# Kernel tuning notes

Hardware: AMD Instinct MI355X
Metric: run time of the kernel (lower is better)

## Reference

```python
import jax, jax.numpy as jnp
import numpy as np

B, T, F, H = 256, 512, 64, 128


def _uniform(key, shape, stdv):
    return jax.random.uniform(key, shape, jnp.float32, -stdv, stdv)


def setup_inputs() -> dict:
    key = jax.random.key(0)
    ks = jax.random.split(key, 24)
    values = jax.random.normal(ks[0], (B, T, F), jnp.float32)
    masks = (jax.random.uniform(ks[1], (B, T, F)) < 0.8).astype(jnp.float32)
    deltas = jax.random.uniform(ks[2], (B, T, F), jnp.float32)
    labels = (jax.random.uniform(ks[3], (B, 1)) < 0.5).astype(jnp.float32)
    is_train = (jax.random.uniform(ks[4], (B, 1)) < 0.8).astype(jnp.float32)
    sH = 1.0 / np.sqrt(H)
    sF = 1.0 / np.sqrt(F)
    # temp_decay_h: Linear F -> H (stdv = 1/sqrt(out) per reset_parameters)
    W_dh = _uniform(ks[5], (H, F), sH); b_dh = _uniform(ks[6], (H,), sH)
    # temp_decay_x: diag F -> F
    W_dx = _uniform(ks[7], (F, F), sF); b_dx = _uniform(ks[8], (F,), sF)
    # hist_reg: Linear H -> F (torch Linear stdv = 1/sqrt(in))
    W_hr = _uniform(ks[9], (F, H), sH); b_hr = _uniform(ks[10], (F,), sH)
    # feat_reg: F -> F with zeroed diagonal mask
    W_fr = _uniform(ks[11], (F, F), sF); b_fr = _uniform(ks[12], (F,), sF)
    # weight_combine: Linear 2F -> F
    s2F = 1.0 / np.sqrt(2 * F)
    W_wc = _uniform(ks[13], (F, 2 * F), s2F); b_wc = _uniform(ks[14], (F,), s2F)
    # LSTMCell(2F, H): torch init uniform(-1/sqrt(H), 1/sqrt(H)), gate order i,f,g,o
    W_ih = _uniform(ks[15], (4 * H, 2 * F), sH); b_ih = _uniform(ks[16], (4 * H,), sH)
    W_hh = _uniform(ks[17], (4 * H, H), sH); b_hh = _uniform(ks[18], (4 * H,), sH)
    # out: Linear H -> 1
    W_out = _uniform(ks[19], (1, H), sH); b_out = _uniform(ks[20], (1,), sH)
    return dict(values=values, masks=masks, deltas=deltas, labels=labels, is_train=is_train,
                W_dh=W_dh, b_dh=b_dh, W_dx=W_dx, b_dx=b_dx, W_hr=W_hr, b_hr=b_hr,
                W_fr=W_fr, b_fr=b_fr, W_wc=W_wc, b_wc=b_wc,
                W_ih=W_ih, b_ih=b_ih, W_hh=W_hh, b_hh=b_hh, W_out=W_out, b_out=b_out)


def _forward(values, masks, deltas, labels, is_train,
             W_dh, b_dh, W_dx, b_dx, W_hr, b_hr, W_fr, b_fr, W_wc, b_wc,
             W_ih, b_ih, W_hh, b_hh, W_out, b_out):
    eps = 1e-5
    w_dx_diag = jnp.diagonal(W_dx)            # diag mask: W * I
    W_fr_m = W_fr * (1.0 - jnp.eye(F, dtype=W_fr.dtype))  # zero diagonal

    def step(carry, xs):
        h, c, x_loss = carry
        x, m, d = xs                           # each [B, F]
        gamma_h = jnp.exp(-jax.nn.relu(d @ W_dh.T + b_dh))   # [B, H]
        gamma_x = jnp.exp(-jax.nn.relu(d * w_dx_diag + b_dx))  # [B, F]
        h = h * gamma_h
        x_h = h @ W_hr.T + b_hr                # [B, F]
        msum = jnp.sum(m) + eps
        x_loss = x_loss + jnp.sum(jnp.abs(x - x_h) * m) / msum
        x_c = m * x + (1.0 - m) * x_h
        z_h = x_c @ W_fr_m.T + b_fr
        x_loss = x_loss + jnp.sum(jnp.abs(x - z_h) * m) / msum
        alpha = jnp.concatenate([gamma_x, m], axis=1) @ W_wc.T + b_wc
        c_h = alpha * z_h + (1.0 - alpha) * x_h
        x_loss = x_loss + jnp.sum(jnp.abs(x - c_h) * m) / msum
        c_c = m * x + (1.0 - m) * c_h
        inp = jnp.concatenate([c_c, m], axis=1)   # [B, 2F]
        gates = inp @ W_ih.T + b_ih + h @ W_hh.T + b_hh  # [B, 4H]
        i, f, g, o = jnp.split(gates, 4, axis=1)
        c = jax.nn.sigmoid(f) * c + jax.nn.sigmoid(i) * jnp.tanh(g)
        h = jax.nn.sigmoid(o) * jnp.tanh(c)
        return (h, c, x_loss), c_c

    h0 = jnp.zeros((values.shape[0], H), values.dtype)
    c0 = jnp.zeros((values.shape[0], H), values.dtype)
    xs = (jnp.swapaxes(values, 0, 1), jnp.swapaxes(masks, 0, 1), jnp.swapaxes(deltas, 0, 1))
    (h, c, x_loss), imps = jax.lax.scan(step, (h0, c0, jnp.float32(0.0)), xs)
    imputations = jnp.swapaxes(imps, 0, 1)     # [B, T, F]
    y_h = h @ W_out.T + b_out                  # [B, 1] logits
    # stable BCE with logits (matches torch reference formula)
    max_val = jnp.maximum(-y_h, 0.0)
    y_l = y_h - y_h * labels + max_val + jnp.log(jnp.exp(-max_val) + jnp.exp(-y_h - max_val))
    y_loss = jnp.sum(y_l * is_train) / (jnp.sum(is_train) + eps)
    loss = x_loss / T + y_loss * 0.3
    predictions = jax.nn.sigmoid(y_h)
    return loss, predictions, imputations


def reference(values, masks, deltas, labels, is_train,
              W_dh, b_dh, W_dx, b_dx, W_hr, b_hr, W_fr, b_fr, W_wc, b_wc,
              W_ih, b_ih, W_hh, b_hh, W_out, b_out):
    return _forward(values, masks, deltas, labels, is_train,
                    W_dh, b_dh, W_dx, b_dx, W_hr, b_hr, W_fr, b_fr, W_wc, b_wc,
                    W_ih, b_ih, W_hh, b_hh, W_out, b_out)
```

## Files before the change

### kernel.cpp

```cpp
#include <hip/hip_runtime.h>
#include <hip/hip_fp16.h>


#define NBATCH 256
#define NT 512
#define NF 64
#define NH 128

#define WHH_OFF   0u
#define WIH_OFF   131072u
#define WHR_OFF   262144u
#define WFR_OFF   278528u
#define INVMS_OFF 286720u
#define ISTR_OFF  288768u
#define GH_OFF    294912u
#define AL_OFF    33849344u

typedef _Float16 half2_t __attribute__((ext_vector_type(2)));

__device__ __forceinline__ unsigned pack2(float a, float b) {
    __half2 h = __floats2half2_rn(a, b);
    return __builtin_bit_cast(unsigned, h);
}

__device__ __forceinline__ float dot2f(unsigned w, unsigned a, float acc) {
#if __has_builtin(__builtin_amdgcn_fdot2)
    return __builtin_amdgcn_fdot2(__builtin_bit_cast(half2_t, w),
                                  __builtin_bit_cast(half2_t, a), acc, false);
#else
    float2 wf = __half22float2(__builtin_bit_cast(__half2, w));
    float2 af = __half22float2(__builtin_bit_cast(__half2, a));
    return acc + wf.x * af.x + wf.y * af.y;
#endif
}

__device__ __forceinline__ float sigm(float x) { return 1.f / (1.f + __expf(-x)); }
__device__ __forceinline__ float tanh_fast(float x) { return 1.f - 2.f / (__expf(2.f * x) + 1.f); }

__global__ __launch_bounds__(256) void prep_w(const float* __restrict__ Whh,
                                              const float* __restrict__ Wih,
                                              const float* __restrict__ Whr,
                                              const float* __restrict__ Wfr,
                                              unsigned* __restrict__ wsu) {
    int o = blockIdx.x * 256 + threadIdx.x;
    float v0, v1;
    if (o < 32768) {
        int c = o & 3, r = (o >> 2) & 511, cb = o >> 11;
        int col = 8 * cb + 2 * c;
        v0 = Whh[r * 128 + col]; v1 = Whh[r * 128 + col + 1];
    } else if (o < 65536) {
        int o2 = o - 32768;
        int c = o2 & 3, r = (o2 >> 2) & 511, cb = o2 >> 11;
        int col = 8 * cb + 2 * c;
        v0 = Wih[r * 128 + col]; v1 = Wih[r * 128 + col + 1];
    } else if (o < 69632) {
        int o3 = o - 65536;
        int c = o3 & 3, f = (o3 >> 2) & 63, cb = o3 >> 8;
        int col = 8 * cb + 2 * c;
        v0 = Whr[f * 128 + col]; v1 = Whr[f * 128 + col + 1];
    } else if (o < 71680) {
        int o4 = o - 69632;
        int c = o4 & 3, f = (o4 >> 2) & 63, cb = o4 >> 8;
        int col = 8 * cb + 2 * c;
        v0 = (col == f) ? 0.f : Wfr[f * 64 + col];
        v1 = (col + 1 == f) ? 0.f : Wfr[f * 64 + col + 1];
    } else {
        return;
    }
    wsu[o] = pack2(v0, v1);
}

__global__ __launch_bounds__(256) void prep_msum(const float* __restrict__ masks,
                                                 const float* __restrict__ is_train,
                                                 float* __restrict__ invms,
                                                 float* __restrict__ inv_istr,
                                                 float* __restrict__ d_out0) {
    __shared__ float red[256];
    int tid = threadIdx.x;
    int t = blockIdx.x;
    if (t < NT) {
        int f = tid & 63, br = tid >> 6;
        float s = 0.f;
        for (int i = 0; i < 64; i++) {
            int b = br + i * 4;
            s += masks[((size_t)b * NT + t) * NF + f];
        }
        red[tid] = s;
        __syncthreads();
        for (int off = 128; off > 0; off >>= 1) {
            if (tid < off) red[tid] += red[tid + off];
            __syncthreads();
        }
        if (tid == 0) invms[t] = 1.f / (red[0] + 1e-5f);
    } else {
        red[tid] = is_train[tid];
        __syncthreads();
        for (int off = 128; off > 0; off >>= 1) {
            if (tid < off) red[tid] += red[tid + off];
            __syncthreads();
        }
        if (tid == 0) {
            *inv_istr = 1.f / (red[0] + 1e-5f);
            *d_out0 = 0.f;
        }
    }
}

__global__ __launch_bounds__(256) void ga_kernel(const float* __restrict__ deltas,
                                                 const float* __restrict__ masks,
                                                 const float* __restrict__ Wdh,
                                                 const float* __restrict__ bdh,
                                                 const float* __restrict__ Wdx,
                                                 const float* __restrict__ bdx,
                                                 const float* __restrict__ Wwc,
                                                 const float* __restrict__ bwc,
                                                 __half* __restrict__ gh_all,
                                                 __half* __restrict__ al_all) {
    __shared__ unsigned wdhpk[32 * 128];
    __shared__ unsigned wwcpk[64 * 64];
    __shared__ float sbdh[128], sbdx[64], swdx[64], sbwc[64];
    __shared__ float dbuf[64];
    __shared__ __align__(16) unsigned dpk[32], gxpk[32], mpk2[32];
    int tid = threadIdx.x;

    for (int o = tid; o < 4096; o += 256) {
        int j = o & 127, k2 = o >> 7;
        wdhpk[o] = pack2(Wdh[j * 64 + 2 * k2], Wdh[j * 64 + 2 * k2 + 1]);
    }
    for (int o = tid; o < 4096; o += 256) {
        int f = o & 63, k2 = o >> 6;
        wwcpk[o] = pack2(Wwc[f * 128 + 2 * k2], Wwc[f * 128 + 2 * k2 + 1]);
    }
    if (tid < 128) sbdh[tid] = bdh[tid];
    if (tid < 64) {
        sbdx[tid] = bdx[tid];
        swdx[tid] = Wdx[tid * 65];
        sbwc[tid] = bwc[tid];
    }
    __syncthreads();

    for (int i = 0; i < 32; i++) {
        int p = blockIdx.x * 32 + i;
        if (tid < 32) {
            float2 dv = ((const float2*)(deltas + (size_t)p * NF))[tid];
            dbuf[2 * tid] = dv.x; dbuf[2 * tid + 1] = dv.y;
            dpk[tid] = pack2(dv.x, dv.y);
        } else if (tid < 64) {
            int q = tid - 32;
            float2 mv = ((const float2*)(masks + (size_t)p * NF))[q];
            mpk2[q] = pack2(mv.x, mv.y);
        }
        __syncthreads();
        if (tid < 64) {
            float gx = __expf(-fmaxf(dbuf[tid] * swdx[tid] + sbdx[tid], 0.f));
            float oth = __shfl_xor(gx, 1);
            if (!(tid & 1)) gxpk[tid >> 1] = pack2(gx, oth);
        }
        __syncthreads();
        if (tid < 128) {
            float a0 = sbdh[tid], a1 = 0.f;
            #pragma unroll
            for (int k8 = 0; k8 < 8; k8++) {
                uint4 dp = *(const uint4*)&dpk[4 * k8];
                a0 = dot2f(wdhpk[(4 * k8 + 0) * 128 + tid], dp.x, a0);
                a1 = dot2f(wdhpk[(4 * k8 + 1) * 128 + tid], dp.y, a1);
                a0 = dot2f(wdhpk[(4 * k8 + 2) * 128 + tid], dp.z, a0);
                a1 = dot2f(wdhpk[(4 * k8 + 3) * 128 + tid], dp.w, a1);
            }
            gh_all[(size_t)p * NH + tid] = __float2half(__expf(-fmaxf(a0 + a1, 0.f)));
        } else if (tid < 192) {
            int f = tid - 128;
            float a0 = sbwc[f], a1 = 0.f;
            #pragma unroll
            for (int k8 = 0; k8 < 8; k8++) {
                uint4 gp = *(const uint4*)&gxpk[4 * k8];
                a0 = dot2f(wwcpk[(4 * k8 + 0) * 64 + f], gp.x, a0);
                a1 = dot2f(wwcpk[(4 * k8 + 1) * 64 + f], gp.y, a1);
                a0 = dot2f(wwcpk[(4 * k8 + 2) * 64 + f], gp.z, a0);
                a1 = dot2f(wwcpk[(4 * k8 + 3) * 64 + f], gp.w, a1);
            }
            #pragma unroll
            for (int k8 = 0; k8 < 8; k8++) {
                uint4 mp = *(const uint4*)&mpk2[4 * k8];
                a0 = dot2f(wwcpk[(32 + 4 * k8 + 0) * 64 + f], mp.x, a0);
                a1 = dot2f(wwcpk[(32 + 4 * k8 + 1) * 64 + f], mp.y, a1);
                a0 = dot2f(wwcpk[(32 + 4 * k8 + 2) * 64 + f], mp.z, a0);
                a1 = dot2f(wwcpk[(32 + 4 * k8 + 3) * 64 + f], mp.w, a1);
            }
            al_all[(size_t)p * NF + f] = __float2half(a0 + a1);
        }
        __syncthreads();
    }
}

__global__ __launch_bounds__(512, 2) void main_kernel(
    const float* __restrict__ values, const float* __restrict__ masks,
    const float* __restrict__ labels, const float* __restrict__ is_train,
    const float* __restrict__ b_hr, const float* __restrict__ b_fr,
    const float* __restrict__ b_ih, const float* __restrict__ b_hh,
    const float* __restrict__ W_out, const float* __restrict__ b_out,
    const uint4* __restrict__ whh_ws, const uint4* __restrict__ wih_ws,
    const uint4* __restrict__ whr_ws, const uint4* __restrict__ wfr_ws,
    const float* __restrict__ invms, const float* __restrict__ inv_istr,
    const __half* __restrict__ gh_all, const __half* __restrict__ al_all,
    float* __restrict__ d_out) {
    __shared__ uint4 whr4[16 * 64];
    __shared__ uint4 wfr4[8 * 64];
    __shared__ float bgate[512];
    __shared__ float sbhr[64], sbfr[64];
    __shared__ float hbuf[128], cbuf[128];
    __shared__ float mbuf[64];
    __shared__ __align__(16) unsigned hpk[64];
    __shared__ __align__(16) unsigned mpk[32], xcpk[32], ccpk[32];
    __shared__ float gates[512];

    const int tid = threadIdx.x;
    const int b = blockIdx.x;

    uint4 whh_r[16], wih_r[16];
    #pragma unroll
    for (int cb = 0; cb < 16; cb++) {
        whh_r[cb] = whh_ws[cb * 512 + tid];
        wih_r[cb] = wih_ws[cb * 512 + tid];
    }
    for (int o = tid; o < 1024; o += 512) whr4[o] = whr_ws[o];
    if (tid < 512) wfr4[tid] = wfr_ws[tid];
    bgate[tid] = b_ih[tid] + b_hh[tid];
    if (tid < 64) { sbhr[tid] = b_hr[tid]; sbfr[tid] = b_fr[tid]; }
    if (tid < 128) { hbuf[tid] = 0.f; cbuf[tid] = 0.f; }
    if (tid < 64) hpk[tid] = 0u;

    const float* vp = values + (size_t)b * NT * NF;
    const float* mp = masks + (size_t)b * NT * NF;
    const __half* alp = al_all + (size_t)b * NT * NF;
    const unsigned* ghu = (const unsigned*)(gh_all + (size_t)b * NT * NH);
    float* imp = d_out + 257 + (size_t)b * NT * NF;

    float lloss = 0.f;
    float xreg = 0.f, mreg = 0.f, xh_reg = 0.f;

    float xn = 0.f, aln = 0.f, invtn = 0.f;
    float2 mn = make_float2(0.f, 0.f);
    unsigned ghn = 0u;
    float alc = 0.f, invtc = 0.f;

    if (tid < 64) {
        xn = vp[tid];
        aln = __half2float(alp[tid]);
        invtn = invms[0];
    } else if (tid < 96) {
        mn = ((const float2*)mp)[tid - 64];
    } else if (tid < 160) {
        ghn = ghu[tid - 96];
    }
    __syncthreads();

    for (int t = 0; t < NT; t++) {
        if (tid < 64) {
            xreg = xn; alc = aln; invtc = invtn;
        } else if (tid < 96) {
            int q = tid - 64;
            mbuf[2 * q] = mn.x; mbuf[2 * q + 1] = mn.y;
            mpk[q] = pack2(mn.x, mn.y);
        } else if (tid < 160) {
            int q = tid - 96;
            float2 g = __half22float2(__builtin_bit_cast(__half2, ghn));
            float h0 = hbuf[2 * q] * g.x;
            float h1 = hbuf[2 * q + 1] * g.y;
            hbuf[2 * q] = h0; hbuf[2 * q + 1] = h1;
            hpk[q] = pack2(h0, h1);
        }
        __syncthreads();

        if (tid < 64) {
            int f = tid;
            mreg = mbuf[f];
            float a0 = sbhr[f], a1 = 0.f;
            #pragma unroll
            for (int k4 = 0; k4 < 16; k4 += 2) {
                uint4 w = whr4[k4 * 64 + f];
                uint4 hp = *(const uint4*)&hpk[4 * k4];
                a0 = dot2f(w.x, hp.x, a0); a0 = dot2f(w.y, hp.y, a0);
                a0 = dot2f(w.z, hp.z, a0); a0 = dot2f(w.w, hp.w, a0);
                uint4 w2 = whr4[(k4 + 1) * 64 + f];
                uint4 hp2 = *(const uint4*)&hpk[4 * k4 + 4];
                a1 = dot2f(w2.x, hp2.x, a1); a1 = dot2f(w2.y, hp2.y, a1);
                a1 = dot2f(w2.z, hp2.z, a1); a1 = dot2f(w2.w, hp2.w, a1);
            }
            xh_reg = a0 + a1;
            float xc = mreg * xreg + (1.f - mreg) * xh_reg;
            float oth = __shfl_xor(xc, 1);
            if (!(f & 1)) xcpk[f >> 1] = pack2(xc, oth);
        }
        __syncthreads();

        if (tid < 64) {
            int f = tid;
            float a0 = sbfr[f], a1 = 0.f;
            #pragma unroll
            for (int k4 = 0; k4 < 8; k4++) {
                uint4 w = wfr4[k4 * 64 + f];
                uint4 xp = *(const uint4*)&xcpk[4 * k4];
                a0 = dot2f(w.x, xp.x, a0); a1 = dot2f(w.y, xp.y, a1);
                a0 = dot2f(w.z, xp.z, a0); a1 = dot2f(w.w, xp.w, a1);
            }
            float zh = a0 + a1;
            float ch = alc * zh + (1.f - alc) * xh_reg;
            float cc = mreg * xreg + (1.f - mreg) * ch;
            imp[t * NF + f] = cc;
            lloss += (fabsf(xreg - xh_reg) + fabsf(xreg - zh) + fabsf(xreg - ch)) * mreg * invtc;
            float oth = __shfl_xor(cc, 1);
            if (!(f & 1)) ccpk[f >> 1] = pack2(cc, oth);
        }
        __syncthreads();

        {
            int tn = (t + 1 < NT) ? (t + 1) : (NT - 1);
            if (tid < 64) {
                xn = vp[tn * NF + tid];
                aln = __half2float(alp[tn * NF + tid]);
                invtn = invms[tn];
            } else if (tid < 96) {
                mn = ((const float2*)(mp + tn * NF))[tid - 64];
            } else if (tid < 160) {
                ghn = ghu[(size_t)tn * 64 + (tid - 96)];
            }

            float a0 = bgate[tid], a1 = 0.f, a2 = 0.f, a3 = 0.f;
            #pragma unroll
            for (int cb = 0; cb < 8; cb++) {
                uint4 ap = *(const uint4*)&ccpk[4 * cb];
                uint4 w = wih_r[cb];
                a0 = dot2f(w.x, ap.x, a0); a1 = dot2f(w.y, ap.y, a1);
                a2 = dot2f(w.z, ap.z, a2); a3 = dot2f(w.w, ap.w, a3);
            }
            #pragma unroll
            for (int cb = 0; cb < 8; cb++) {
                uint4 ap = *(const uint4*)&mpk[4 * cb];
                uint4 w = wih_r[8 + cb];
                a0 = dot2f(w.x, ap.x, a0); a1 = dot2f(w.y, ap.y, a1);
                a2 = dot2f(w.z, ap.z, a2); a3 = dot2f(w.w, ap.w, a3);
            }
            #pragma unroll
            for (int k4 = 0; k4 < 16; k4++) {
                uint4 hp = *(const uint4*)&hpk[4 * k4];
                uint4 w = whh_r[k4];
                a0 = dot2f(w.x, hp.x, a0); a1 = dot2f(w.y, hp.y, a1);
                a2 = dot2f(w.z, hp.z, a2); a3 = dot2f(w.w, hp.w, a3);
            }
            gates[tid] = (a0 + a1) + (a2 + a3);
        }
        __syncthreads();

        if (tid < 128) {
            float gi = gates[tid], gf = gates[128 + tid];
            float gg = gates[256 + tid], go = gates[384 + tid];
            float cn = sigm(gf) * cbuf[tid] + sigm(gi) * tanh_fast(gg);
            cbuf[tid] = cn;
            hbuf[tid] = sigm(go) * tanh_fast(cn);
        }
        __syncthreads();
    }

    if (tid < 64) {
        float ll = lloss;
        float yp = hbuf[tid] * W_out[tid] + hbuf[64 + tid] * W_out[64 + tid];
        #pragma unroll
        for (int off = 32; off > 0; off >>= 1) {
            ll += __shfl_down(ll, off);
            yp += __shfl_down(yp, off);
        }
        if (tid == 0) {
            float yh = yp + b_out[0];
            d_out[1 + b] = 1.f / (1.f + expf(-yh));
            float lab = labels[b], istr = is_train[b];
            float maxv = fmaxf(-yh, 0.f);
            float yl = yh - yh * lab + maxv + logf(expf(-maxv) + expf(-yh - maxv));
            atomicAdd(d_out, ll * (1.f / (float)NT) + 0.3f * yl * istr * (*inv_istr));
        }
    }
}

extern "C" void kernel_launch(void* const* d_in, const int* in_sizes, int n_in,
                              void* d_out, int out_size, void* d_ws, size_t ws_size,
                              hipStream_t stream) {
    const float* values = (const float*)d_in[0];
    const float* masks = (const float*)d_in[1];
    const float* deltas = (const float*)d_in[2];
    const float* labels = (const float*)d_in[3];
    const float* is_train = (const float*)d_in[4];
    const float* W_dh = (const float*)d_in[5];
    const float* b_dh = (const float*)d_in[6];
    const float* W_dx = (const float*)d_in[7];
    const float* b_dx = (const float*)d_in[8];
    const float* W_hr = (const float*)d_in[9];
    const float* b_hr = (const float*)d_in[10];
    const float* W_fr = (const float*)d_in[11];
    const float* b_fr = (const float*)d_in[12];
    const float* W_wc = (const float*)d_in[13];
    const float* b_wc = (const float*)d_in[14];
    const float* W_ih = (const float*)d_in[15];
    const float* b_ih = (const float*)d_in[16];
    const float* W_hh = (const float*)d_in[17];
    const float* b_hh = (const float*)d_in[18];
    const float* W_out = (const float*)d_in[19];
    const float* b_out = (const float*)d_in[20];

    char* ws = (char*)d_ws;
    unsigned* wsu = (unsigned*)d_ws;
    const uint4* whh_ws = (const uint4*)(ws + WHH_OFF);
    const uint4* wih_ws = (const uint4*)(ws + WIH_OFF);
    const uint4* whr_ws = (const uint4*)(ws + WHR_OFF);
    const uint4* wfr_ws = (const uint4*)(ws + WFR_OFF);
    float* invms = (float*)(ws + INVMS_OFF);
    float* inv_istr = (float*)(ws + ISTR_OFF);
    __half* gh_all = (__half*)(ws + GH_OFF);
    __half* al_all = (__half*)(ws + AL_OFF);
    float* out_f = (float*)d_out;

    prep_w<<<280, 256, 0, stream>>>(W_hh, W_ih, W_hr, W_fr, wsu);
    prep_msum<<<513, 256, 0, stream>>>(masks, is_train, invms, inv_istr, out_f);
    ga_kernel<<<4096, 256, 0, stream>>>(deltas, masks, W_dh, b_dh, W_dx, b_dx,
                                        W_wc, b_wc, gh_all, al_all);
    main_kernel<<<NBATCH, 512, 0, stream>>>(values, masks, labels, is_train,
                                            b_hr, b_fr, b_ih, b_hh, W_out, b_out,
                                            whh_ws, wih_ws, whr_ws, wfr_ws,
                                            invms, inv_istr, gh_all, al_all, out_f);
}
```

Baseline: 1.376 ms.

## Compute LSTM gates with MFMA and split regression dot products across all threads

The LSTM gate matrix-vector product, previously done with per-thread fdot2 over register-resident weights, now uses 16x16x32 f16 MFMA instructions. The combined W_ih|W_hh weights are pre-swizzled into A-fragment layout so they can stay in registers. The hidden-state part of the gates is issued early to overlap with the regression stages. The hist_reg and feat_reg dot products are split across all 8 waves, with partial sums reduced in shared memory at the cost of an extra barrier. Cell state moves into registers, the decayed h is packed directly, next-step loads are prefetched at loop top, and ga_kernel gets more blocks with fewer positions each.

```diff
diff --git a/kernel.cpp b/kernel.cpp
--- a/kernel.cpp
+++ b/kernel.cpp
@@ -7,8 +7,7 @@
 #define NF 64
 #define NH 128
 
-#define WHH_OFF   0u
-#define WIH_OFF   131072u
+#define AFRAG_OFF 0u
 #define WHR_OFF   262144u
 #define WFR_OFF   278528u
 #define INVMS_OFF 286720u
@@ -17,6 +16,8 @@
 #define AL_OFF    33849344u
 
 typedef _Float16 half2_t __attribute__((ext_vector_type(2)));
+typedef _Float16 half8_t __attribute__((ext_vector_type(8)));
+typedef float float4_t __attribute__((ext_vector_type(4)));
 
 __device__ __forceinline__ unsigned pack2(float a, float b) {
     __half2 h = __floats2half2_rn(a, b);
@@ -34,25 +35,31 @@
 #endif
 }
 
+__device__ __forceinline__ float4_t mfma16(half8_t a, half8_t b, float4_t c) {
+    return __builtin_amdgcn_mfma_f32_16x16x32_f16(a, b, c, 0, 0, 0);
+}
+
 __device__ __forceinline__ float sigm(float x) { return 1.f / (1.f + __expf(-x)); }
 __device__ __forceinline__ float tanh_fast(float x) { return 1.f - 2.f / (__expf(2.f * x) + 1.f); }
 
-__global__ __launch_bounds__(256) void prep_w(const float* __restrict__ Whh,
-                                              const float* __restrict__ Wih,
+__global__ __launch_bounds__(256) void prep_w(const float* __restrict__ Wih,
+                                              const float* __restrict__ Whh,
                                               const float* __restrict__ Whr,
                                               const float* __restrict__ Wfr,
                                               unsigned* __restrict__ wsu) {
     int o = blockIdx.x * 256 + threadIdx.x;
     float v0, v1;
-    if (o < 32768) {
-        int c = o & 3, r = (o >> 2) & 511, cb = o >> 11;
-        int col = 8 * cb + 2 * c;
-        v0 = Whh[r * 128 + col]; v1 = Whh[r * 128 + col + 1];
-    } else if (o < 65536) {
-        int o2 = o - 32768;
-        int c = o2 & 3, r = (o2 >> 2) & 511, cb = o2 >> 11;
-        int col = 8 * cb + 2 * c;
-        v0 = Wih[r * 128 + col]; v1 = Wih[r * 128 + col + 1];
+    if (o < 65536) {
+        int comp = o & 3;
+        int u4 = o >> 2;
+        int lane = u4 & 63;
+        int tile = u4 >> 6;
+        int kt = tile & 7, rt = (tile >> 3) & 3, w = tile >> 5;
+        int row = 64 * w + 16 * rt + (lane & 15);
+        int kp = 16 * kt + ((lane >> 4) << 2) + comp;
+        int k0 = 2 * kp;
+        if (k0 < 128) { v0 = Wih[row * 128 + k0]; v1 = Wih[row * 128 + k0 + 1]; }
+        else          { v0 = Whh[row * 128 + k0 - 128]; v1 = Whh[row * 128 + k0 - 127]; }
     } else if (o < 69632) {
         int o3 = o - 65536;
         int c = o3 & 3, f = (o3 >> 2) & 63, cb = o3 >> 8;
@@ -139,8 +146,8 @@
     }
     __syncthreads();
 
-    for (int i = 0; i < 32; i++) {
-        int p = blockIdx.x * 32 + i;
+    for (int i = 0; i < 8; i++) {
+        int p = blockIdx.x * 8 + i;
         if (tid < 32) {
             float2 dv = ((const float2*)(deltas + (size_t)p * NF))[tid];
             dbuf[2 * tid] = dv.x; dbuf[2 * tid + 1] = dv.y;
@@ -199,172 +206,196 @@
     const float* __restrict__ b_hr, const float* __restrict__ b_fr,
     const float* __restrict__ b_ih, const float* __restrict__ b_hh,
     const float* __restrict__ W_out, const float* __restrict__ b_out,
-    const uint4* __restrict__ whh_ws, const uint4* __restrict__ wih_ws,
-    const uint4* __restrict__ whr_ws, const uint4* __restrict__ wfr_ws,
+    const uint4* __restrict__ afrag_ws, const uint4* __restrict__ whr_ws,
+    const uint4* __restrict__ wfr_ws,
     const float* __restrict__ invms, const float* __restrict__ inv_istr,
     const __half* __restrict__ gh_all, const __half* __restrict__ al_all,
     float* __restrict__ d_out) {
-    __shared__ uint4 whr4[16 * 64];
-    __shared__ uint4 wfr4[8 * 64];
-    __shared__ float bgate[512];
+    __shared__ __align__(16) uint4 whr4u[16 * 64];
+    __shared__ __align__(16) uint4 wfr4u[8 * 64];
+    __shared__ float bpart[512], cpart[512], gates[512];
+    __shared__ float xbuf[64], mbuf[64], albuf[64];
     __shared__ float sbhr[64], sbfr[64];
-    __shared__ float hbuf[128], cbuf[128];
-    __shared__ float mbuf[64];
     __shared__ __align__(16) unsigned hpk[64];
     __shared__ __align__(16) unsigned mpk[32], xcpk[32], ccpk[32];
-    __shared__ float gates[512];
+    __shared__ float sinv[1];
 
     const int tid = threadIdx.x;
     const int b = blockIdx.x;
-
-    uint4 whh_r[16], wih_r[16];
+    const int f = tid & 63;
+    const int s = tid >> 6;
+    const int q4 = (tid >> 4) & 3;
+
+    uint4 afr[4][8];
     #pragma unroll
-    for (int cb = 0; cb < 16; cb++) {
-        whh_r[cb] = whh_ws[cb * 512 + tid];
-        wih_r[cb] = wih_ws[cb * 512 + tid];
-    }
-    for (int o = tid; o < 1024; o += 512) whr4[o] = whr_ws[o];
-    if (tid < 512) wfr4[tid] = wfr_ws[tid];
-    bgate[tid] = b_ih[tid] + b_hh[tid];
+    for (int rt = 0; rt < 4; rt++)
+        #pragma unroll
+        for (int kt = 0; kt < 8; kt++) {
+            afr[rt][kt] = afrag_ws[(((s * 4 + rt) * 8) + kt) * 64 + f];
+            asm volatile("" : "+v"(afr[rt][kt].x), "+v"(afr[rt][kt].y),
+                              "+v"(afr[rt][kt].z), "+v"(afr[rt][kt].w));
+        }
+
+    float4_t bias_r[4];
+    #pragma unroll
+    for (int rt = 0; rt < 4; rt++)
+        #pragma unroll
+        for (int reg = 0; reg < 4; reg++) {
+            int row = 64 * s + 16 * rt + 4 * q4 + reg;
+            bias_r[rt][reg] = b_ih[row] + b_hh[row];
+        }
+
+    for (int o = tid; o < 1024; o += 512) whr4u[o] = whr_ws[o];
+    if (tid < 512) wfr4u[tid] = wfr_ws[tid];
     if (tid < 64) { sbhr[tid] = b_hr[tid]; sbfr[tid] = b_fr[tid]; }
-    if (tid < 128) { hbuf[tid] = 0.f; cbuf[tid] = 0.f; }
-    if (tid < 64) hpk[tid] = 0u;
 
     const float* vp = values + (size_t)b * NT * NF;
     const float* mp = masks + (size_t)b * NT * NF;
     const __half* alp = al_all + (size_t)b * NT * NF;
-    const unsigned* ghu = (const unsigned*)(gh_all + (size_t)b * NT * NH);
+    const __half* ghp = gh_all + (size_t)b * NT * NH;
     float* imp = d_out + 257 + (size_t)b * NT * NF;
 
+    if (tid < 64) {
+        float x0 = vp[tid];
+        float m0 = mp[tid];
+        xbuf[tid] = x0; mbuf[tid] = m0;
+        albuf[tid] = __half2float(alp[tid]);
+        float m1 = __shfl_xor(m0, 1);
+        if (!(tid & 1)) mpk[tid >> 1] = pack2(m0, m1);
+        hpk[tid] = 0u;
+    }
+    if (tid == 64) sinv[0] = invms[0];
+    __syncthreads();
+
+    float creg = 0.f, hn = 0.f;
     float lloss = 0.f;
-    float xreg = 0.f, mreg = 0.f, xh_reg = 0.f;
-
-    float xn = 0.f, aln = 0.f, invtn = 0.f;
-    float2 mn = make_float2(0.f, 0.f);
-    unsigned ghn = 0u;
-    float alc = 0.f, invtc = 0.f;
-
-    if (tid < 64) {
-        xn = vp[tid];
-        aln = __half2float(alp[tid]);
-        invtn = invms[0];
-    } else if (tid < 96) {
-        mn = ((const float2*)mp)[tid - 64];
-    } else if (tid < 160) {
-        ghn = ghu[tid - 96];
-    }
-    __syncthreads();
 
     for (int t = 0; t < NT; t++) {
+        int tn = (t + 1 < NT) ? (t + 1) : (NT - 1);
+        __half ghn = __float2half(0.f);
+        float2 mn2 = make_float2(0.f, 0.f);
+        float xn = 0.f, aln = 0.f, invtn = 0.f;
+        if (tid < 128) ghn = ghp[(size_t)tn * NH + tid];
+        else if (tid < 160) mn2 = ((const float2*)(mp + tn * NF))[tid - 128];
+        else if (tid < 256 && tid >= 192) xn = vp[tn * NF + (tid - 192)];
+        else if (tid >= 256 && tid < 320) aln = __half2float(alp[tn * NF + (tid - 256)]);
+        else if (tid == 320) invtn = invms[tn];
+
+        float4_t acc[4];
+        {
+            half8_t bh[4];
+            #pragma unroll
+            for (int j = 0; j < 4; j++)
+                bh[j] = *((const half8_t*)&hpk[16 * j + 4 * q4]);
+            #pragma unroll
+            for (int rt = 0; rt < 4; rt++) {
+                acc[rt] = bias_r[rt];
+                #pragma unroll
+                for (int j = 0; j < 4; j++)
+                    acc[rt] = mfma16(__builtin_bit_cast(half8_t, afr[rt][4 + j]), bh[j], acc[rt]);
+            }
+        }
+
+        {
+            uint4 w0 = whr4u[(2 * s) * 64 + f];
+            uint4 w1 = whr4u[(2 * s + 1) * 64 + f];
+            uint4 h0 = *(const uint4*)&hpk[8 * s];
+            uint4 h1 = *(const uint4*)&hpk[8 * s + 4];
+            float p0 = 0.f, p1 = 0.f;
+            p0 = dot2f(w0.x, h0.x, p0); p1 = dot2f(w0.y, h0.y, p1);
+            p0 = dot2f(w0.z, h0.z, p0); p1 = dot2f(w0.w, h0.w, p1);
+            p0 = dot2f(w1.x, h1.x, p0); p1 = dot2f(w1.y, h1.y, p1);
+            p0 = dot2f(w1.z, h1.z, p0); p1 = dot2f(w1.w, h1.w, p1);
+            bpart[s * 64 + f] = p0 + p1;
+        }
+        __syncthreads();
+
+        float xreg = 0.f, mreg = 0.f, invt = 0.f, xh_keep = 0.f;
         if (tid < 64) {
-            xreg = xn; alc = aln; invtc = invtn;
-        } else if (tid < 96) {
-            int q = tid - 64;
-            mbuf[2 * q] = mn.x; mbuf[2 * q + 1] = mn.y;
-            mpk[q] = pack2(mn.x, mn.y);
-        } else if (tid < 160) {
-            int q = tid - 96;
-            float2 g = __half22float2(__builtin_bit_cast(__half2, ghn));
-            float h0 = hbuf[2 * q] * g.x;
-            float h1 = hbuf[2 * q + 1] * g.y;
-            hbuf[2 * q] = h0; hbuf[2 * q + 1] = h1;
-            hpk[q] = pack2(h0, h1);
-        }
-        __syncthreads();
-
-        if (tid < 64) {
-            int f = tid;
-            mreg = mbuf[f];
-            float a0 = sbhr[f], a1 = 0.f;
-            #pragma unroll
-            for (int k4 = 0; k4 < 16; k4 += 2) {
-                uint4 w = whr4[k4 * 64 + f];
-                uint4 hp = *(const uint4*)&hpk[4 * k4];
-                a0 = dot2f(w.x, hp.x, a0); a0 = dot2f(w.y, hp.y, a0);
-                a0 = dot2f(w.z, hp.z, a0); a0 = dot2f(w.w, hp.w, a0);
-                uint4 w2 = whr4[(k4 + 1) * 64 + f];
-                uint4 hp2 = *(const uint4*)&hpk[4 * k4 + 4];
-                a1 = dot2f(w2.x, hp2.x, a1); a1 = dot2f(w2.y, hp2.y, a1);
-                a1 = dot2f(w2.z, hp2.z, a1); a1 = dot2f(w2.w, hp2.w, a1);
-            }
-            xh_reg = a0 + a1;
-            float xc = mreg * xreg + (1.f - mreg) * xh_reg;
+            float xh = sbhr[f];
+            #pragma unroll
+            for (int s2 = 0; s2 < 8; s2++) xh += bpart[s2 * 64 + f];
+            xreg = xbuf[f]; mreg = mbuf[f]; invt = sinv[0];
+            xh_keep = xh;
+            float xc = mreg * xreg + (1.f - mreg) * xh;
+            lloss += fabsf(xreg - xh) * mreg * invt;
             float oth = __shfl_xor(xc, 1);
             if (!(f & 1)) xcpk[f >> 1] = pack2(xc, oth);
         }
         __syncthreads();
 
+        {
+            uint4 w = wfr4u[s * 64 + f];
+            uint4 xp = *(const uint4*)&xcpk[4 * s];
+            float p0 = 0.f, p1 = 0.f;
+            p0 = dot2f(w.x, xp.x, p0); p1 = dot2f(w.y, xp.y, p1);
+            p0 = dot2f(w.z, xp.z, p0); p1 = dot2f(w.w, xp.w, p1);
+            cpart[s * 64 + f] = p0 + p1;
+        }
+        __syncthreads();
+
         if (tid < 64) {
-            int f = tid;
-            float a0 = sbfr[f], a1 = 0.f;
-            #pragma unroll
-            for (int k4 = 0; k4 < 8; k4++) {
-                uint4 w = wfr4[k4 * 64 + f];
-                uint4 xp = *(const uint4*)&xcpk[4 * k4];
-                a0 = dot2f(w.x, xp.x, a0); a1 = dot2f(w.y, xp.y, a1);
-                a0 = dot2f(w.z, xp.z, a0); a1 = dot2f(w.w, xp.w, a1);
-            }
-            float zh = a0 + a1;
-            float ch = alc * zh + (1.f - alc) * xh_reg;
+            float zh = sbfr[f];
+            #pragma unroll
+            for (int s2 = 0; s2 < 8; s2++) zh += cpart[s2 * 64 + f];
+            float al = albuf[f];
+            float ch = al * zh + (1.f - al) * xh_keep;
             float cc = mreg * xreg + (1.f - mreg) * ch;
             imp[t * NF + f] = cc;
-            lloss += (fabsf(xreg - xh_reg) + fabsf(xreg - zh) + fabsf(xreg - ch)) * mreg * invtc;
+            lloss += (fabsf(xreg - zh) + fabsf(xreg - ch)) * mreg * invt;
             float oth = __shfl_xor(cc, 1);
             if (!(f & 1)) ccpk[f >> 1] = pack2(cc, oth);
         }
         __syncthreads();
 
         {
-            int tn = (t + 1 < NT) ? (t + 1) : (NT - 1);
-            if (tid < 64) {
-                xn = vp[tn * NF + tid];
-                aln = __half2float(alp[tn * NF + tid]);
-                invtn = invms[tn];
-            } else if (tid < 96) {
-                mn = ((const float2*)(mp + tn * NF))[tid - 64];
-            } else if (tid < 160) {
-                ghn = ghu[(size_t)tn * 64 + (tid - 96)];
-            }
-
-            float a0 = bgate[tid], a1 = 0.f, a2 = 0.f, a3 = 0.f;
-            #pragma unroll
-            for (int cb = 0; cb < 8; cb++) {
-                uint4 ap = *(const uint4*)&ccpk[4 * cb];
-                uint4 w = wih_r[cb];
-                a0 = dot2f(w.x, ap.x, a0); a1 = dot2f(w.y, ap.y, a1);
-                a2 = dot2f(w.z, ap.z, a2); a3 = dot2f(w.w, ap.w, a3);
-            }
-            #pragma unroll
-            for (int cb = 0; cb < 8; cb++) {
-                uint4 ap = *(const uint4*)&mpk[4 * cb];
-                uint4 w = wih_r[8 + cb];
-                a0 = dot2f(w.x, ap.x, a0); a1 = dot2f(w.y, ap.y, a1);
-                a2 = dot2f(w.z, ap.z, a2); a3 = dot2f(w.w, ap.w, a3);
-            }
-            #pragma unroll
-            for (int k4 = 0; k4 < 16; k4++) {
-                uint4 hp = *(const uint4*)&hpk[4 * k4];
-                uint4 w = whh_r[k4];
-                a0 = dot2f(w.x, hp.x, a0); a1 = dot2f(w.y, hp.y, a1);
-                a2 = dot2f(w.z, hp.z, a2); a3 = dot2f(w.w, hp.w, a3);
-            }
-            gates[tid] = (a0 + a1) + (a2 + a3);
+            half8_t bc[4];
+            bc[0] = *((const half8_t*)&ccpk[4 * q4]);
+            bc[1] = *((const half8_t*)&ccpk[16 + 4 * q4]);
+            bc[2] = *((const half8_t*)&mpk[4 * q4]);
+            bc[3] = *((const half8_t*)&mpk[16 + 4 * q4]);
+            #pragma unroll
+            for (int rt = 0; rt < 4; rt++) {
+                #pragma unroll
+                for (int j = 0; j < 4; j++)
+                    acc[rt] = mfma16(__builtin_bit_cast(half8_t, afr[rt][j]), bc[j], acc[rt]);
+            }
+            if ((tid & 15) == 0) {
+                #pragma unroll
+                for (int rt = 0; rt < 4; rt++)
+                    *((float4_t*)&gates[64 * s + 16 * rt + 4 * q4]) = acc[rt];
+            }
         }
         __syncthreads();
 
         if (tid < 128) {
             float gi = gates[tid], gf = gates[128 + tid];
             float gg = gates[256 + tid], go = gates[384 + tid];
-            float cn = sigm(gf) * cbuf[tid] + sigm(gi) * tanh_fast(gg);
-            cbuf[tid] = cn;
-            hbuf[tid] = sigm(go) * tanh_fast(cn);
-        }
-        __syncthreads();
-    }
-
+            float cn = sigm(gf) * creg + sigm(gi) * tanh_fast(gg);
+            creg = cn;
+            hn = sigm(go) * tanh_fast(cn);
+            float hd = hn * __half2float(ghn);
+            float oth = __shfl_xor(hd, 1);
+            if (!(tid & 1)) hpk[tid >> 1] = pack2(hd, oth);
+        } else if (tid < 160) {
+            int q = tid - 128;
+            mbuf[2 * q] = mn2.x; mbuf[2 * q + 1] = mn2.y;
+            mpk[q] = pack2(mn2.x, mn2.y);
+        } else if (tid >= 192 && tid < 256) {
+            xbuf[tid - 192] = xn;
+        } else if (tid >= 256 && tid < 320) {
+            albuf[tid - 256] = aln;
+        } else if (tid == 320) {
+            sinv[0] = invtn;
+        }
+        __syncthreads();
+    }
+
+    if (tid < 128) bpart[tid] = hn * W_out[tid];
+    __syncthreads();
     if (tid < 64) {
+        float yp = bpart[tid] + bpart[tid + 64];
         float ll = lloss;
-        float yp = hbuf[tid] * W_out[tid] + hbuf[64 + tid] * W_out[64 + tid];
         #pragma unroll
         for (int off = 32; off > 0; off >>= 1) {
             ll += __shfl_down(ll, off);
@@ -408,8 +439,7 @@
 
     char* ws = (char*)d_ws;
     unsigned* wsu = (unsigned*)d_ws;
-    const uint4* whh_ws = (const uint4*)(ws + WHH_OFF);
-    const uint4* wih_ws = (const uint4*)(ws + WIH_OFF);
+    const uint4* afrag_ws = (const uint4*)(ws + AFRAG_OFF);
     const uint4* whr_ws = (const uint4*)(ws + WHR_OFF);
     const uint4* wfr_ws = (const uint4*)(ws + WFR_OFF);
     float* invms = (float*)(ws + INVMS_OFF);
@@ -418,12 +448,12 @@
     __half* al_all = (__half*)(ws + AL_OFF);
     float* out_f = (float*)d_out;
 
-    prep_w<<<280, 256, 0, stream>>>(W_hh, W_ih, W_hr, W_fr, wsu);
+    prep_w<<<280, 256, 0, stream>>>(W_ih, W_hh, W_hr, W_fr, wsu);
     prep_msum<<<513, 256, 0, stream>>>(masks, is_train, invms, inv_istr, out_f);
-    ga_kernel<<<4096, 256, 0, stream>>>(deltas, masks, W_dh, b_dh, W_dx, b_dx,
-                                        W_wc, b_wc, gh_all, al_all);
+    ga_kernel<<<16384, 256, 0, stream>>>(deltas, masks, W_dh, b_dh, W_dx, b_dx,
+                                         W_wc, b_wc, gh_all, al_all);
     main_kernel<<<NBATCH, 512, 0, stream>>>(values, masks, labels, is_train,
                                             b_hr, b_fr, b_ih, b_hh, W_out, b_out,
-                                            whh_ws, wih_ws, whr_ws, wfr_ws,
+                                            afrag_ws, whr_ws, wfr_ws,
                                             invms, inv_istr, gh_all, al_all, out_f);
 }
```

Measured after the change: 1.509 ms. 1.1x slower.
